# Optimization experiments

Hardware: AMD Instinct MI355X
Metric: run time of the kernel (lower is better)

Reference implementation:

```python
import jax, jax.numpy as jnp
import numpy as np

B = 512
EPS = 1e-5


def _coords():
    # cvt_coord(i) = [(i//5 - 2)/2, (i%5 - 2)/2] on a 5x5 grid
    c = np.array([[(i // 5 - 2) / 2.0, (i % 5 - 2) / 2.0] for i in range(25)], dtype=np.float32)
    return jnp.asarray(c)  # [25, 2]


def setup_inputs() -> dict:
    key = jax.random.key(0)
    ks = jax.random.split(key, 32)
    d = {
        'img': jax.random.normal(ks[0], (B, 3, 75, 75), jnp.float32),
        'qst': jax.random.normal(ks[1], (B, 11), jnp.float32),
    }
    # conv backbone params
    cin = [3, 24, 24, 24]
    for l in range(4):
        d[f'conv_w{l+1}'] = jax.random.normal(ks[2 + l], (24, cin[l], 3, 3), jnp.float32) * 0.1
        d[f'conv_b{l+1}'] = jnp.zeros((24,), jnp.float32)
        d[f'bn_g{l+1}'] = 1.0 + 0.05 * jax.random.normal(ks[6 + l], (24,), jnp.float32)
        d[f'bn_b{l+1}'] = 0.05 * jax.random.normal(ks[10 + l], (24,), jnp.float32)
    # g MLP (63->256, 256->256 x3)
    d['g_w1'] = jax.random.normal(ks[14], (256, 63), jnp.float32) * 0.05
    d['g_b1'] = jnp.zeros((256,), jnp.float32)
    for l in (2, 3, 4):
        d[f'g_w{l}'] = jax.random.normal(ks[13 + l], (256, 256), jnp.float32) * 0.05
        d[f'g_b{l}'] = jnp.zeros((256,), jnp.float32)
    # f MLP and output head
    d['f_w1'] = jax.random.normal(ks[20], (256, 256), jnp.float32) * 0.05
    d['f_b1'] = jnp.zeros((256,), jnp.float32)
    d['fc2_w'] = jax.random.normal(ks[21], (256, 256), jnp.float32) * 0.05
    d['fc2_b'] = jnp.zeros((256,), jnp.float32)
    d['fc3_w'] = jax.random.normal(ks[22], (10, 256), jnp.float32) * 0.05
    d['fc3_b'] = jnp.zeros((10,), jnp.float32)
    return d


def _conv_bn(x, w, b, g, be):
    y = jax.lax.conv_general_dilated(x, w, (2, 2), [(1, 1), (1, 1)],
                                     dimension_numbers=('NCHW', 'OIHW', 'NCHW'))
    y = jax.nn.relu(y + b[None, :, None, None])
    # BatchNorm2d with batch statistics (training-mode forward)
    mu = jnp.mean(y, axis=(0, 2, 3), keepdims=True)
    var = jnp.var(y, axis=(0, 2, 3), keepdims=True)
    return (y - mu) * jax.lax.rsqrt(var + EPS) * g[None, :, None, None] + be[None, :, None, None]


def _lin(x, w, b):
    return x @ w.T + b


def reference(img, qst,
              conv_w1, conv_b1, bn_g1, bn_b1,
              conv_w2, conv_b2, bn_g2, bn_b2,
              conv_w3, conv_b3, bn_g3, bn_b3,
              conv_w4, conv_b4, bn_g4, bn_b4,
              g_w1, g_b1, g_w2, g_b2, g_w3, g_b3, g_w4, g_b4,
              f_w1, f_b1, fc2_w, fc2_b, fc3_w, fc3_b):
    x = _conv_bn(img, conv_w1, conv_b1, bn_g1, bn_b1)
    x = _conv_bn(x, conv_w2, conv_b2, bn_g2, bn_b2)
    x = _conv_bn(x, conv_w3, conv_b3, bn_g3, bn_b3)
    x = _conv_bn(x, conv_w4, conv_b4, bn_g4, bn_b4)  # [B, 24, 5, 5]
    mb = x.shape[0]
    x_flat = x.reshape(mb, 24, 25).transpose(0, 2, 1)  # [B, 25, 24]
    coords = jnp.broadcast_to(_coords()[None], (mb, 25, 2))
    x_flat = jnp.concatenate([x_flat, coords], axis=2)  # [B, 25, 26]
    # all-pairs: pair (p, q) -> concat(obj_q, obj_p, qst)
    xj = jnp.concatenate([x_flat, jnp.broadcast_to(qst[:, None, :], (mb, 25, 11))], axis=2)  # [B,25,37]
    x_i = jnp.broadcast_to(x_flat[:, None, :, :], (mb, 25, 25, 26))
    x_j = jnp.broadcast_to(xj[:, :, None, :], (mb, 25, 25, 37))
    x_full = jnp.concatenate([x_i, x_j], axis=3).reshape(mb * 625, 63)
    h = jax.nn.relu(_lin(x_full, g_w1, g_b1))
    h = jax.nn.relu(_lin(h, g_w2, g_b2))
    h = jax.nn.relu(_lin(h, g_w3, g_b3))
    h = jax.nn.relu(_lin(h, g_w4, g_b4))
    x_g = h.reshape(mb, 625, 256).sum(axis=1)  # [B, 256]
    x_f = jax.nn.relu(_lin(x_g, f_w1, f_b1))
    x_f = jax.nn.relu(_lin(x_f, fc2_w, fc2_b))  # (dropout omitted: eval/deterministic)
    logits = _lin(x_f, fc3_w, fc3_b)
    return jax.nn.log_softmax(logits, axis=-1)
```

## Files before the change

### kernel.cpp

```cpp
#include <hip/hip_runtime.h>
#include <hip/hip_bf16.h>

#define EPS 1e-5f

typedef _Float16 half_t;
typedef __attribute__((ext_vector_type(8))) _Float16 h16x8;
typedef __attribute__((ext_vector_type(4))) _Float16 h16x4;
typedef __attribute__((ext_vector_type(4))) float f32x4;

__device__ __forceinline__ float relu_f(float x) { return x > 0.f ? x : 0.f; }

#define OFF_Y1   0
#define OFF_Y2   17743872
#define OFF_Y3   22179840
#define OFF_Y4   23408640
#define OFF_ST   23715840
#define OFF_WHL  23718912
#define OFF_A    0
#define OFF_BV   3276800
#define OFF_XG   6553600
#define OFF_WHL2 8871936

__global__ __launch_bounds__(256) void k_prep(const float* w2, const float* w3,
                                              const float* w4, half_t* whl, float* stats) {
    int idx = blockIdx.x * 256 + threadIdx.x;
    if (idx < 3072) stats[idx] = 0.f;
    int l = idx >> 16, e = idx & 65535;
    const float* w = (l == 0) ? w2 : (l == 1) ? w3 : w4;
    float v = w[e];
    int c = e >> 8, k = e & 255;
    int o = ((c >> 4) * 8 + (k >> 5)) * 512 + ((k >> 3) & 3) * 128 + (c & 15) * 8 + (k & 7);
    whl[l * 65536 + o] = (half_t)v;
}

__global__ __launch_bounds__(256) void k_prep2(const float* w2, half_t* whl2) {
    int idx = blockIdx.x * 256 + threadIdx.x;
    int ntile = idx / 3584, r = idx % 3584;
    int ks = r / 512, w = r % 512;
    int quad = w / 128, l15 = (w >> 3) & 15, j = w & 7;
    int k = ks * 32 + quad * 8 + j;
    int oc = ntile * 16 + l15;
    float v = 0.f;
    if (k < 216 && oc < 24) {
        int tap = k / 24, ic = k % 24;
        v = w2[(oc * 24 + ic) * 9 + tap];
    }
    whl2[idx] = (half_t)v;
}

__global__ __launch_bounds__(256, 2) void k_conv1(const float* img, const float* w,
                                                  const float* bias, half_t* y1, float* ostats) {
    __shared__ float wl[648], bl[24], red[4][48];
    int tid = threadIdx.x;
    if (tid < 24) bl[tid] = bias[tid];
    for (int i = tid; i < 648; i += 256) wl[i] = w[i];
    __syncthreads();
    int idx = blockIdx.x * 256 + tid;
    int b2 = idx / 1444, rem = idx % 1444;
    int b0 = b2 * 2;
    int oh = rem / 38, ow = rem % 38;
    float acc0[24], acc1[24];
#pragma unroll
    for (int o = 0; o < 24; ++o) { acc0[o] = bl[o]; acc1[o] = bl[o]; }
    for (int ic = 0; ic < 3; ++ic) {
        float p0[9], p1[9];
#pragma unroll
        for (int kh = 0; kh < 3; ++kh) {
            int ih = oh * 2 - 1 + kh;
#pragma unroll
            for (int kw = 0; kw < 3; ++kw) {
                int iw = ow * 2 - 1 + kw;
                bool ok = (unsigned)ih < 75u && (unsigned)iw < 75u;
                p0[kh * 3 + kw] = ok ? img[((b0 * 3 + ic) * 75 + ih) * 75 + iw] : 0.f;
                p1[kh * 3 + kw] = ok ? img[(((b0 + 1) * 3 + ic) * 75 + ih) * 75 + iw] : 0.f;
            }
        }
#pragma unroll
        for (int o = 0; o < 24; ++o)
#pragma unroll
            for (int t = 0; t < 9; ++t) {
                float wv = wl[(o * 3 + ic) * 9 + t];
                acc0[o] += wv * p0[t];
                acc1[o] += wv * p1[t];
            }
    }
#pragma unroll
    for (int o = 0; o < 24; ++o) { acc0[o] = relu_f(acc0[o]); acc1[o] = relu_f(acc1[o]); }
#pragma unroll
    for (int g = 0; g < 3; ++g) {
        h16x8 a, c;
#pragma unroll
        for (int j = 0; j < 8; ++j) { a[j] = (half_t)acc0[g * 8 + j]; c[j] = (half_t)acc1[g * 8 + j]; }
        *(h16x8*)&y1[((long)(b0) * 1444 + rem) * 24 + g * 8] = a;
        *(h16x8*)&y1[((long)(b0 + 1) * 1444 + rem) * 24 + g * 8] = c;
    }
    int wave = tid >> 6;
#pragma unroll
    for (int o = 0; o < 24; ++o) {
        float v = acc0[o] + acc1[o];
        float v2 = acc0[o] * acc0[o] + acc1[o] * acc1[o];
#pragma unroll
        for (int off = 1; off < 64; off <<= 1) { v += __shfl_xor(v, off); v2 += __shfl_xor(v2, off); }
        if ((tid & 63) == 0) { red[wave][o] = v; red[wave][24 + o] = v2; }
    }
    __syncthreads();
    if (tid < 48)
        atomicAdd(&ostats[(blockIdx.x & 15) * 48 + tid],
                  red[0][tid] + red[1][tid] + red[2][tid] + red[3][tid]);
}

__global__ __launch_bounds__(256) void k_conv2(const half_t* yin, const half_t* whl2,
                                               const float* bias, const float* instats,
                                               const float* bng, const float* bnb,
                                               float* yout, float* ostats) {
    __shared__ half_t yL[34672];
    __shared__ half_t wf[7168];
    __shared__ float outL[8856];
    __shared__ float scs[24], shs[24], bl[24], red[4][48];
    int tid = threadIdx.x;
    int b = blockIdx.x;
    if (tid < 24) {
        float s = 0.f, s2 = 0.f;
#pragma unroll
        for (int k = 0; k < 16; ++k) { s += instats[k * 48 + tid]; s2 += instats[k * 48 + 24 + tid]; }
        float mu = s * (1.f / 739328.f);
        float var = s2 * (1.f / 739328.f) - mu * mu;
        float sca = bng[tid] * rsqrtf(var + EPS);
        scs[tid] = sca; shs[tid] = bnb[tid] - mu * sca;
        bl[tid] = bias[tid];
    }
    if (tid < 16) yL[34656 + tid] = (half_t)0.f;
    for (int i = tid; i < 896; i += 256)
        ((h16x8*)wf)[i] = ((const h16x8*)whl2)[i];
    __syncthreads();
    const half_t* ybase = yin + (long)b * 34656;
    for (int i = tid; i < 4332; i += 256) {
        h16x8 v = *(const h16x8*)&ybase[i * 8];
        int ch0 = (i % 3) * 8;
        h16x8 o;
#pragma unroll
        for (int j = 0; j < 8; ++j)
            o[j] = (half_t)((float)v[j] * scs[ch0 + j] + shs[ch0 + j]);
        *(h16x8*)&yL[i * 8] = o;
    }
    __syncthreads();
    int wv = tid >> 6, lane = tid & 63, quad = lane >> 4, l15 = lane & 15;
    float bb0 = bl[l15];
    float bb1 = (l15 < 8) ? bl[16 + l15] : 0.f;
    float s0 = 0.f, q0 = 0.f, s1 = 0.f, q1 = 0.f;
    int t0 = wv * 6, t1 = t0 + 6; if (t1 > 23) t1 = 23;
#pragma unroll 1
    for (int t = t0; t < t1; ++t) {
        int px0 = t * 16;
        int pxa = px0 + l15; if (pxa > 360) pxa = 360;
        int oh = pxa / 19, ow = pxa % 19;
        f32x4 a0 = (f32x4){0.f, 0.f, 0.f, 0.f};
        f32x4 a1 = (f32x4){0.f, 0.f, 0.f, 0.f};
#pragma unroll
        for (int ks = 0; ks < 7; ++ks) {
            int k0 = ks * 32 + quad * 8;
            int tap = k0 / 24, ic0 = k0 - tap * 24;
            int kh = tap / 3, kw = tap - kh * 3;
            int ih = oh * 2 - 1 + kh, iw = ow * 2 - 1 + kw;
            bool val = (tap < 9) && ((unsigned)ih < 38u) && ((unsigned)iw < 38u);
            int aoff = val ? ((ih * 38 + iw) * 24 + ic0) : 34656;
            h16x8 af = *(const h16x8*)&yL[aoff];
            h16x8 w0 = *(const h16x8*)&wf[ks * 512 + quad * 128 + l15 * 8];
            h16x8 w1 = *(const h16x8*)&wf[3584 + ks * 512 + quad * 128 + l15 * 8];
            a0 = __builtin_amdgcn_mfma_f32_16x16x32_f16(af, w0, a0, 0, 0, 0);
            a1 = __builtin_amdgcn_mfma_f32_16x16x32_f16(af, w1, a1, 0, 0, 0);
        }
#pragma unroll
        for (int v = 0; v < 4; ++v) {
            int p = px0 + quad * 4 + v;
            bool pv = p < 361;
            float x0 = relu_f(a0[v] + bb0);
            float x1 = relu_f(a1[v] + bb1);
            outL[l15 * 369 + p] = x0;
            if (l15 < 8) outL[(16 + l15) * 369 + p] = x1;
            if (pv) {
                s0 += x0; q0 += x0 * x0;
                if (l15 < 8) { s1 += x1; q1 += x1 * x1; }
            }
        }
    }
    s0 += __shfl_xor(s0, 16); s0 += __shfl_xor(s0, 32);
    q0 += __shfl_xor(q0, 16); q0 += __shfl_xor(q0, 32);
    s1 += __shfl_xor(s1, 16); s1 += __shfl_xor(s1, 32);
    q1 += __shfl_xor(q1, 16); q1 += __shfl_xor(q1, 32);
    if (quad == 0) {
        red[wv][l15] = s0; red[wv][24 + l15] = q0;
        if (l15 < 8) { red[wv][16 + l15] = s1; red[wv][40 + l15] = q1; }
    }
    __syncthreads();
    float* yo = yout + (long)b * 8664;
    for (int i = tid; i < 8664; i += 256) {
        int oc = i / 361, p = i - oc * 361;
        yo[i] = outL[oc * 369 + p];
    }
    if (tid < 48)
        atomicAdd(&ostats[(blockIdx.x & 15) * 48 + tid],
                  red[0][tid] + red[1][tid] + red[2][tid] + red[3][tid]);
}

__global__ __launch_bounds__(256) void k_conv(const float* yin, const float* w,
                                              const float* bias, const float* instats,
                                              const float* bng, const float* bnb,
                                              float* yout, float* ostats,
                                              int Hin, int Hout, float invN) {
    __shared__ float wl[5184], bl[24], sc[24], sh[24], red[4][48];
    int tid = threadIdx.x;
    if (tid < 24) {
        float s = 0.f, s2 = 0.f;
#pragma unroll
        for (int k = 0; k < 16; ++k) { s += instats[k * 48 + tid]; s2 += instats[k * 48 + 24 + tid]; }
        float mu = s * invN;
        float var = s2 * invN - mu * mu;
        float sca = bng[tid] * rsqrtf(var + EPS);
        sc[tid] = sca; sh[tid] = bnb[tid] - mu * sca;
        bl[tid] = bias[tid];
    }
    for (int i = tid; i < 5184; i += 256) wl[i] = w[i];
    __syncthreads();
    int idx = blockIdx.x * 256 + tid;
    int HWo = Hout * Hout;
    int b = idx / HWo, rem = idx % HWo;
    int oh = rem / Hout, ow = rem % Hout;
    float acc[24];
#pragma unroll
    for (int o = 0; o < 24; ++o) acc[o] = bl[o];
    for (int ic = 0; ic < 24; ++ic) {
        float patch[9];
        float scc = sc[ic], shc = sh[ic];
#pragma unroll
        for (int kh = 0; kh < 3; ++kh) {
            int ih = oh * 2 - 1 + kh;
#pragma unroll
            for (int kw = 0; kw < 3; ++kw) {
                int iw = ow * 2 - 1 + kw;
                bool ok = (unsigned)ih < (unsigned)Hin && (unsigned)iw < (unsigned)Hin;
                patch[kh * 3 + kw] = ok ? yin[((b * 24 + ic) * Hin + ih) * Hin + iw] * scc + shc : 0.f;
            }
        }
#pragma unroll
        for (int o = 0; o < 24; ++o)
#pragma unroll
            for (int t = 0; t < 9; ++t) acc[o] += wl[(o * 24 + ic) * 9 + t] * patch[t];
    }
    int wave = tid >> 6;
#pragma unroll
    for (int o = 0; o < 24; ++o) {
        acc[o] = relu_f(acc[o]);
        yout[(b * 24 + o) * HWo + rem] = acc[o];
        float v = acc[o], v2 = v * v;
#pragma unroll
        for (int off = 1; off < 64; off <<= 1) { v += __shfl_xor(v, off); v2 += __shfl_xor(v2, off); }
        if ((tid & 63) == 0) { red[wave][o] = v; red[wave][24 + o] = v2; }
    }
    __syncthreads();
    if (tid < 48)
        atomicAdd(&ostats[(blockIdx.x & 15) * 48 + tid],
                  red[0][tid] + red[1][tid] + red[2][tid] + red[3][tid]);
}

__global__ __launch_bounds__(256) void k_obj(const float* y4, const float* qst,
                                             const float* w1, const float* b1,
                                             const float* instats, const float* bng,
                                             const float* bnb, float* A, float* Bv, float* xg) {
    int b = blockIdx.x, tid = threadIdx.x;
    __shared__ float w1l[16128];
    __shared__ float objs[25][28];
    __shared__ float sc[24], sh[24], q[11];
    xg[b * 256 + tid] = 0.f;
    for (int i = tid; i < 16128; i += 256) w1l[i] = w1[i];
    if (tid < 24) {
        float s = 0.f, s2 = 0.f;
#pragma unroll
        for (int k = 0; k < 16; ++k) { s += instats[k * 48 + tid]; s2 += instats[k * 48 + 24 + tid]; }
        float mu = s * (1.f / 12800.f);
        float var = s2 * (1.f / 12800.f) - mu * mu;
        float sca = bng[tid] * rsqrtf(var + EPS);
        sc[tid] = sca; sh[tid] = bnb[tid] - mu * sca;
    }
    if (tid < 11) q[tid] = qst[b * 11 + tid];
    __syncthreads();
    for (int i = tid; i < 600; i += 256) {
        int c = i / 25, p = i % 25;
        objs[p][c] = y4[b * 600 + i] * sc[c] + sh[c];
    }
    if (tid < 25) { objs[tid][24] = ((tid / 5) - 2) * 0.5f; objs[tid][25] = ((tid % 5) - 2) * 0.5f; }
    __syncthreads();
    float wr[63];
#pragma unroll
    for (int k = 0; k < 63; ++k) wr[k] = w1l[tid * 63 + k];
    float qdot = b1[tid];
#pragma unroll
    for (int j = 0; j < 11; ++j) qdot += wr[52 + j] * q[j];
#pragma unroll 1
    for (int p = 0; p < 25; ++p) {
        float a = 0.f, bv = qdot;
#pragma unroll
        for (int k = 0; k < 26; ++k) { a += wr[k] * objs[p][k]; bv += wr[26 + k] * objs[p][k]; }
        A[(b * 25 + p) * 256 + tid] = a;
        Bv[(b * 25 + p) * 256 + tid] = bv;
    }
}

#define GSTEP(C0,C1,C2,C3,N0,N1,N2,N3,KS,LKS,DOLOAD) do {                                   \
    int ko = (KS) * 32 + quad * 8;                                                          \
    h16x8 b0 = *(const h16x8*)&hr[0 * 4224 + ko];                                           \
    h16x8 b1 = *(const h16x8*)&hr[1 * 4224 + ko];                                           \
    h16x8 b2 = *(const h16x8*)&hr[2 * 4224 + ko];                                           \
    h16x8 b3 = *(const h16x8*)&hr[3 * 4224 + ko];                                           \
    if (DOLOAD) {                                                                           \
        N0 = *(const h16x8*)&W[0 * 4096 + (LKS) * 512];                                     \
        N1 = *(const h16x8*)&W[1 * 4096 + (LKS) * 512];                                     \
        N2 = *(const h16x8*)&W[2 * 4096 + (LKS) * 512];                                     \
        N3 = *(const h16x8*)&W[3 * 4096 + (LKS) * 512];                                     \
    }                                                                                       \
    __builtin_amdgcn_s_setprio(1);                                                          \
    acc[0][0] = __builtin_amdgcn_mfma_f32_16x16x32_f16(C0, b0, acc[0][0], 0, 0, 0);         \
    acc[1][0] = __builtin_amdgcn_mfma_f32_16x16x32_f16(C1, b0, acc[1][0], 0, 0, 0);         \
    acc[2][0] = __builtin_amdgcn_mfma_f32_16x16x32_f16(C2, b0, acc[2][0], 0, 0, 0);         \
    acc[3][0] = __builtin_amdgcn_mfma_f32_16x16x32_f16(C3, b0, acc[3][0], 0, 0, 0);         \
    acc[0][1] = __builtin_amdgcn_mfma_f32_16x16x32_f16(C0, b1, acc[0][1], 0, 0, 0);         \
    acc[1][1] = __builtin_amdgcn_mfma_f32_16x16x32_f16(C1, b1, acc[1][1], 0, 0, 0);         \
    acc[2][1] = __builtin_amdgcn_mfma_f32_16x16x32_f16(C2, b1, acc[2][1], 0, 0, 0);         \
    acc[3][1] = __builtin_amdgcn_mfma_f32_16x16x32_f16(C3, b1, acc[3][1], 0, 0, 0);         \
    acc[0][2] = __builtin_amdgcn_mfma_f32_16x16x32_f16(C0, b2, acc[0][2], 0, 0, 0);         \
    acc[1][2] = __builtin_amdgcn_mfma_f32_16x16x32_f16(C1, b2, acc[1][2], 0, 0, 0);         \
    acc[2][2] = __builtin_amdgcn_mfma_f32_16x16x32_f16(C2, b2, acc[2][2], 0, 0, 0);         \
    acc[3][2] = __builtin_amdgcn_mfma_f32_16x16x32_f16(C3, b2, acc[3][2], 0, 0, 0);         \
    acc[0][3] = __builtin_amdgcn_mfma_f32_16x16x32_f16(C0, b3, acc[0][3], 0, 0, 0);         \
    acc[1][3] = __builtin_amdgcn_mfma_f32_16x16x32_f16(C1, b3, acc[1][3], 0, 0, 0);         \
    acc[2][3] = __builtin_amdgcn_mfma_f32_16x16x32_f16(C2, b3, acc[2][3], 0, 0, 0);         \
    acc[3][3] = __builtin_amdgcn_mfma_f32_16x16x32_f16(C3, b3, acc[3][3], 0, 0, 0);         \
    __builtin_amdgcn_s_setprio(0);                                                          \
} while (0)

__global__ __launch_bounds__(256, 3) void k_g(const float* A, const float* Bv, const half_t* whl,
                                              const float* gb2, const float* gb3,
                                              const float* gb4, float* xg) {
    __shared__ alignas(16) half_t h[64 * 264];
    __shared__ float biasL[3][256];
    int tid = threadIdx.x;
    int lb = (blockIdx.x & 7) * 640 + (blockIdx.x >> 3);
    int b = lb / 10, t = lb % 10;
    int r0 = t * 64;
    int rmax = 625 - r0; if (rmax > 64) rmax = 64;
    biasL[0][tid] = gb2[tid];
    biasL[1][tid] = gb3[tid];
    biasL[2][tid] = gb4[tid];
    const float* Ab = A + b * 6400;
    const float* Bb = Bv + b * 6400;
#pragma unroll
    for (int it = 0; it < 16; ++it) {
        int r = it * 4 + (tid >> 6);
        int rs = __builtin_amdgcn_readfirstlane(r);
        int pr = r0 + rs; if (pr > 624) pr = 624;
        int i = pr % 25, j = pr / 25;
        int c4 = (tid & 63) << 2;
        float4 av = *(const float4*)&Ab[i * 256 + c4];
        float4 bv = *(const float4*)&Bb[j * 256 + c4];
        h16x4 hv = {(half_t)relu_f(av.x + bv.x), (half_t)relu_f(av.y + bv.y),
                    (half_t)relu_f(av.z + bv.z), (half_t)relu_f(av.w + bv.w)};
        *(h16x4*)&h[r * 264 + c4] = hv;
    }
    __syncthreads();
    int cg = tid >> 6, lane = tid & 63;
    int quad = lane >> 4, l15 = lane & 15;
    const half_t* hr = h + l15 * 264;
    const half_t* Wl = whl + (cg * 4) * 8 * 512 + lane * 8;
#pragma unroll 1
    for (int layer = 0; layer < 3; ++layer) {
        const half_t* W = Wl + layer * 65536;
        f32x4 acc[4][4];
#pragma unroll
        for (int mi = 0; mi < 4; ++mi)
#pragma unroll
            for (int nt = 0; nt < 4; ++nt) acc[mi][nt] = (f32x4){0.f, 0.f, 0.f, 0.f};
        h16x8 wA0 = *(const h16x8*)&W[0 * 4096];
        h16x8 wA1 = *(const h16x8*)&W[1 * 4096];
        h16x8 wA2 = *(const h16x8*)&W[2 * 4096];
        h16x8 wA3 = *(const h16x8*)&W[3 * 4096];
        h16x8 wB0 = *(const h16x8*)&W[0 * 4096 + 512];
        h16x8 wB1 = *(const h16x8*)&W[1 * 4096 + 512];
        h16x8 wB2 = *(const h16x8*)&W[2 * 4096 + 512];
        h16x8 wB3 = *(const h16x8*)&W[3 * 4096 + 512];
        h16x8 wC0, wC1, wC2, wC3;
        GSTEP(wA0, wA1, wA2, wA3, wC0, wC1, wC2, wC3, 0, 2, 1);
        GSTEP(wB0, wB1, wB2, wB3, wA0, wA1, wA2, wA3, 1, 3, 1);
        GSTEP(wC0, wC1, wC2, wC3, wB0, wB1, wB2, wB3, 2, 4, 1);
        GSTEP(wA0, wA1, wA2, wA3, wC0, wC1, wC2, wC3, 3, 5, 1);
        GSTEP(wB0, wB1, wB2, wB3, wA0, wA1, wA2, wA3, 4, 6, 1);
        GSTEP(wC0, wC1, wC2, wC3, wB0, wB1, wB2, wB3, 5, 7, 1);
        GSTEP(wA0, wA1, wA2, wA3, wA0, wA1, wA2, wA3, 6, 0, 0);
        GSTEP(wB0, wB1, wB2, wB3, wB0, wB1, wB2, wB3, 7, 0, 0);
        __syncthreads();
        if (layer < 2) {
#pragma unroll
            for (int mi = 0; mi < 4; ++mi) {
                int c0 = cg * 64 + mi * 16 + quad * 4;
#pragma unroll
                for (int nt = 0; nt < 4; ++nt) {
                    int row = nt * 16 + l15;
                    h16x4 hv;
#pragma unroll
                    for (int v = 0; v < 4; ++v)
                        hv[v] = (half_t)relu_f(acc[mi][nt][v] + biasL[layer][c0 + v]);
                    *(h16x4*)&h[row * 264 + c0] = hv;
                }
            }
            __syncthreads();
        } else {
#pragma unroll
            for (int mi = 0; mi < 4; ++mi) {
                int c0 = cg * 64 + mi * 16 + quad * 4;
#pragma unroll
                for (int v = 0; v < 4; ++v) {
                    float s = 0.f;
#pragma unroll
                    for (int nt = 0; nt < 4; ++nt) {
                        int row = nt * 16 + l15;
                        float x = relu_f(acc[mi][nt][v] + biasL[2][c0 + v]);
                        if (row < rmax) s += x;
                    }
                    s += __shfl_xor(s, 1);
                    s += __shfl_xor(s, 2);
                    s += __shfl_xor(s, 4);
                    s += __shfl_xor(s, 8);
                    if (l15 == 0) atomicAdd(&xg[b * 256 + c0 + v], s);
                }
            }
        }
    }
}

__global__ __launch_bounds__(256) void k_f(const float* xg, const float* fw1, const float* fb1,
                                           const float* fw2, const float* fb2,
                                           const float* fw3, const float* fb3, float* out) {
    int b0 = blockIdx.x * 2, tid = threadIdx.x;
    __shared__ float xb[2][256], h1[2][256], l10[2][10], red[2];
    xb[0][tid] = xg[b0 * 256 + tid];
    xb[1][tid] = xg[(b0 + 1) * 256 + tid];
    __syncthreads();
    float s0 = fb1[tid], s1 = s0;
    {
        const float4* wr = (const float4*)&fw1[tid * 256];
        const float4* x0 = (const float4*)xb[0];
        const float4* x1 = (const float4*)xb[1];
#pragma unroll 8
        for (int k = 0; k < 64; ++k) {
            float4 w = wr[k], a = x0[k], c = x1[k];
            s0 += w.x * a.x + w.y * a.y + w.z * a.z + w.w * a.w;
            s1 += w.x * c.x + w.y * c.y + w.z * c.z + w.w * c.w;
        }
    }
    h1[0][tid] = relu_f(s0);
    h1[1][tid] = relu_f(s1);
    __syncthreads();
    s0 = fb2[tid]; s1 = s0;
    {
        const float4* wr = (const float4*)&fw2[tid * 256];
        const float4* x0 = (const float4*)h1[0];
        const float4* x1 = (const float4*)h1[1];
#pragma unroll 8
        for (int k = 0; k < 64; ++k) {
            float4 w = wr[k], a = x0[k], c = x1[k];
            s0 += w.x * a.x + w.y * a.y + w.z * a.z + w.w * a.w;
            s1 += w.x * c.x + w.y * c.y + w.z * c.z + w.w * c.w;
        }
    }
    __syncthreads();
    xb[0][tid] = relu_f(s0);
    xb[1][tid] = relu_f(s1);
    __syncthreads();
    if (tid < 20) {
        int bb = tid / 10, o = tid % 10;
        float v = fb3[o];
        const float4* wr = (const float4*)&fw3[o * 256];
        const float4* hv = (const float4*)xb[bb];
#pragma unroll 8
        for (int k = 0; k < 64; ++k) {
            float4 w = wr[k], x = hv[k];
            v += w.x * x.x + w.y * x.y + w.z * x.z + w.w * x.w;
        }
        l10[bb][o] = v;
    }
    __syncthreads();
    if (tid < 2) {
        float m = l10[tid][0];
        for (int i = 1; i < 10; ++i) m = fmaxf(m, l10[tid][i]);
        float e = 0.f;
        for (int i = 0; i < 10; ++i) e += expf(l10[tid][i] - m);
        red[tid] = m + logf(e);
    }
    __syncthreads();
    if (tid < 20) {
        int bb = tid / 10, o = tid % 10;
        out[(b0 + bb) * 10 + o] = l10[bb][o] - red[bb];
    }
}

extern "C" void kernel_launch(void* const* d_in, const int* in_sizes, int n_in,
                              void* d_out, int out_size, void* d_ws, size_t ws_size,
                              hipStream_t stream) {
    const float* img = (const float*)d_in[0];
    const float* qst = (const float*)d_in[1];
    const float* cw[4] = {(const float*)d_in[2], (const float*)d_in[6],
                          (const float*)d_in[10], (const float*)d_in[14]};
    const float* cb[4] = {(const float*)d_in[3], (const float*)d_in[7],
                          (const float*)d_in[11], (const float*)d_in[15]};
    const float* bg[4] = {(const float*)d_in[4], (const float*)d_in[8],
                          (const float*)d_in[12], (const float*)d_in[16]};
    const float* bb[4] = {(const float*)d_in[5], (const float*)d_in[9],
                          (const float*)d_in[13], (const float*)d_in[17]};
    const float* gw1 = (const float*)d_in[18];
    const float* gb1 = (const float*)d_in[19];
    const float* gw2 = (const float*)d_in[20];
    const float* gb2 = (const float*)d_in[21];
    const float* gw3 = (const float*)d_in[22];
    const float* gb3 = (const float*)d_in[23];
    const float* gw4 = (const float*)d_in[24];
    const float* gb4 = (const float*)d_in[25];
    const float* fw1 = (const float*)d_in[26];
    const float* fb1 = (const float*)d_in[27];
    const float* fw2 = (const float*)d_in[28];
    const float* fb2 = (const float*)d_in[29];
    const float* fw3 = (const float*)d_in[30];
    const float* fb3 = (const float*)d_in[31];

    float* ws = (float*)d_ws;
    half_t* y1 = (half_t*)(ws + OFF_Y1);
    float* y2 = ws + OFF_Y2;
    float* y3 = ws + OFF_Y3;
    float* y4 = ws + OFF_Y4;
    float* st = ws + OFF_ST;
    half_t* whl = (half_t*)(ws + OFF_WHL);
    half_t* whl2 = (half_t*)(ws + OFF_WHL2);
    float* A = ws + OFF_A;
    float* Bv = ws + OFF_BV;
    float* xg = ws + OFF_XG;
    float* out = (float*)d_out;

    k_prep<<<768, 256, 0, stream>>>(gw2, gw3, gw4, whl, st);
    k_prep2<<<28, 256, 0, stream>>>(cw[1], whl2);
    k_conv1<<<1444, 256, 0, stream>>>(img, cw[0], cb[0], y1, st + 0 * 768);
    k_conv2<<<512, 256, 0, stream>>>(y1, whl2, cb[1], st + 0 * 768, bg[0], bb[0], y2,
                                     st + 1 * 768);
    k_conv<<<200, 256, 0, stream>>>(y2, cw[2], cb[2], st + 1 * 768, bg[1], bb[1], y3,
                                    st + 2 * 768, 19, 10, 1.f / 184832.f);
    k_conv<<<50, 256, 0, stream>>>(y3, cw[3], cb[3], st + 2 * 768, bg[2], bb[2], y4,
                                   st + 3 * 768, 10, 5, 1.f / 51200.f);
    k_obj<<<512, 256, 0, stream>>>(y4, qst, gw1, gb1, st + 3 * 768, bg[3], bb[3], A, Bv, xg);
    k_g<<<5120, 256, 0, stream>>>(A, Bv, whl, gb2, gb3, gb4, xg);
    k_f<<<256, 256, 0, stream>>>(xg, fw1, fb1, fw2, fb2, fw3, fb3, out);
}
```

Baseline: 517.4 us.

## Split conv2 by row halves, shrink conv3/4 blocks, merge prep kernels

Folds k_prep2 into k_prep to drop one launch. Splits k_conv2 into two blocks per image, each covering half the output rows with halo rows staged in LDS, and writes outputs straight to global instead of through an LDS staging buffer. This cuts LDS use and doubles the block count. Relaunches conv3/conv4 with smaller blocks (128 and 64 threads) for more parallelism, vectorizes the w1 load in k_obj, and raises k_g occupancy to 4 blocks per CU. The trade-offs are uncoalesced direct stores in conv2 and register pressure from the tighter k_g launch bound.

```diff
diff --git a/kernel.cpp b/kernel.cpp
--- a/kernel.cpp
+++ b/kernel.cpp
@@ -22,9 +22,23 @@
 #define OFF_WHL2 8871936
 
 __global__ __launch_bounds__(256) void k_prep(const float* w2, const float* w3,
-                                              const float* w4, half_t* whl, float* stats) {
+                                              const float* w4, half_t* whl, float* stats,
+                                              const float* cw2, half_t* whl2) {
     int idx = blockIdx.x * 256 + threadIdx.x;
     if (idx < 3072) stats[idx] = 0.f;
+    if (blockIdx.x < 28) {
+        int ntile = idx / 3584, r = idx % 3584;
+        int ks = r / 512, w = r % 512;
+        int quad = w / 128, l15 = (w >> 3) & 15, j = w & 7;
+        int k = ks * 32 + quad * 8 + j;
+        int oc = ntile * 16 + l15;
+        float v = 0.f;
+        if (k < 216 && oc < 24) {
+            int tap = k / 24, ic = k % 24;
+            v = cw2[(oc * 24 + ic) * 9 + tap];
+        }
+        whl2[idx] = (half_t)v;
+    }
     int l = idx >> 16, e = idx & 65535;
     const float* w = (l == 0) ? w2 : (l == 1) ? w3 : w4;
     float v = w[e];
@@ -33,21 +47,6 @@
     whl[l * 65536 + o] = (half_t)v;
 }
 
-__global__ __launch_bounds__(256) void k_prep2(const float* w2, half_t* whl2) {
-    int idx = blockIdx.x * 256 + threadIdx.x;
-    int ntile = idx / 3584, r = idx % 3584;
-    int ks = r / 512, w = r % 512;
-    int quad = w / 128, l15 = (w >> 3) & 15, j = w & 7;
-    int k = ks * 32 + quad * 8 + j;
-    int oc = ntile * 16 + l15;
-    float v = 0.f;
-    if (k < 216 && oc < 24) {
-        int tap = k / 24, ic = k % 24;
-        v = w2[(oc * 24 + ic) * 9 + tap];
-    }
-    whl2[idx] = (half_t)v;
-}
-
 __global__ __launch_bounds__(256, 2) void k_conv1(const float* img, const float* w,
                                                   const float* bias, half_t* y1, float* ostats) {
     __shared__ float wl[648], bl[24], red[4][48];
@@ -113,12 +112,15 @@
                                                const float* bias, const float* instats,
                                                const float* bng, const float* bnb,
                                                float* yout, float* ostats) {
-    __shared__ half_t yL[34672];
+    __shared__ half_t yL[19168];
     __shared__ half_t wf[7168];
-    __shared__ float outL[8856];
     __shared__ float scs[24], shs[24], bl[24], red[4][48];
     int tid = threadIdx.x;
-    int b = blockIdx.x;
+    int b = blockIdx.x >> 1, hh = blockIdx.x & 1;
+    int oh0 = hh * 10;
+    int NR = hh ? 9 : 10;
+    int NPX = NR * 19;
+    int ihbase = oh0 * 2 - 1;
     if (tid < 24) {
         float s = 0.f, s2 = 0.f;
 #pragma unroll
@@ -129,18 +131,25 @@
         scs[tid] = sca; shs[tid] = bnb[tid] - mu * sca;
         bl[tid] = bias[tid];
     }
-    if (tid < 16) yL[34656 + tid] = (half_t)0.f;
+    if (tid < 16) yL[19152 + tid] = (half_t)0.f;
     for (int i = tid; i < 896; i += 256)
         ((h16x8*)wf)[i] = ((const h16x8*)whl2)[i];
     __syncthreads();
     const half_t* ybase = yin + (long)b * 34656;
-    for (int i = tid; i < 4332; i += 256) {
-        h16x8 v = *(const h16x8*)&ybase[i * 8];
-        int ch0 = (i % 3) * 8;
+    for (int i = tid; i < 2394; i += 256) {
+        int li = i / 114, rem = i - li * 114;
+        int ih = ihbase + li;
         h16x8 o;
-#pragma unroll
-        for (int j = 0; j < 8; ++j)
-            o[j] = (half_t)((float)v[j] * scs[ch0 + j] + shs[ch0 + j]);
+        if ((unsigned)ih < 38u) {
+            h16x8 v = *(const h16x8*)&ybase[(ih * 114 + rem) * 8];
+            int ch0 = (rem % 3) * 8;
+#pragma unroll
+            for (int j = 0; j < 8; ++j)
+                o[j] = (half_t)((float)v[j] * scs[ch0 + j] + shs[ch0 + j]);
+        } else {
+#pragma unroll
+            for (int j = 0; j < 8; ++j) o[j] = (half_t)0.f;
+        }
         *(h16x8*)&yL[i * 8] = o;
     }
     __syncthreads();
@@ -148,12 +157,12 @@
     float bb0 = bl[l15];
     float bb1 = (l15 < 8) ? bl[16 + l15] : 0.f;
     float s0 = 0.f, q0 = 0.f, s1 = 0.f, q1 = 0.f;
-    int t0 = wv * 6, t1 = t0 + 6; if (t1 > 23) t1 = 23;
+    int ntiles = (NPX + 15) >> 4;
 #pragma unroll 1
-    for (int t = t0; t < t1; ++t) {
+    for (int t = wv; t < ntiles; t += 4) {
         int px0 = t * 16;
-        int pxa = px0 + l15; if (pxa > 360) pxa = 360;
-        int oh = pxa / 19, ow = pxa % 19;
+        int pxa = px0 + l15; if (pxa > NPX - 1) pxa = NPX - 1;
+        int lr = pxa / 19, ow = pxa % 19;
         f32x4 a0 = (f32x4){0.f, 0.f, 0.f, 0.f};
         f32x4 a1 = (f32x4){0.f, 0.f, 0.f, 0.f};
 #pragma unroll
@@ -161,9 +170,11 @@
             int k0 = ks * 32 + quad * 8;
             int tap = k0 / 24, ic0 = k0 - tap * 24;
             int kh = tap / 3, kw = tap - kh * 3;
-            int ih = oh * 2 - 1 + kh, iw = ow * 2 - 1 + kw;
-            bool val = (tap < 9) && ((unsigned)ih < 38u) && ((unsigned)iw < 38u);
-            int aoff = val ? ((ih * 38 + iw) * 24 + ic0) : 34656;
+            int li = 2 * lr + kh;
+            int ihg = ihbase + li;
+            int iw = ow * 2 - 1 + kw;
+            bool val = (tap < 9) && ((unsigned)ihg < 38u) && ((unsigned)iw < 38u);
+            int aoff = val ? ((li * 38 + iw) * 24 + ic0) : 19152;
             h16x8 af = *(const h16x8*)&yL[aoff];
             h16x8 w0 = *(const h16x8*)&wf[ks * 512 + quad * 128 + l15 * 8];
             h16x8 w1 = *(const h16x8*)&wf[3584 + ks * 512 + quad * 128 + l15 * 8];
@@ -173,14 +184,16 @@
 #pragma unroll
         for (int v = 0; v < 4; ++v) {
             int p = px0 + quad * 4 + v;
-            bool pv = p < 361;
-            float x0 = relu_f(a0[v] + bb0);
-            float x1 = relu_f(a1[v] + bb1);
-            outL[l15 * 369 + p] = x0;
-            if (l15 < 8) outL[(16 + l15) * 369 + p] = x1;
-            if (pv) {
+            if (p < NPX) {
+                int pg = oh0 * 19 + p;
+                float x0 = relu_f(a0[v] + bb0);
+                yout[((long)b * 24 + l15) * 361 + pg] = x0;
                 s0 += x0; q0 += x0 * x0;
-                if (l15 < 8) { s1 += x1; q1 += x1 * x1; }
+                if (l15 < 8) {
+                    float x1 = relu_f(a1[v] + bb1);
+                    yout[((long)b * 24 + 16 + l15) * 361 + pg] = x1;
+                    s1 += x1; q1 += x1 * x1;
+                }
             }
         }
     }
@@ -193,11 +206,6 @@
         if (l15 < 8) { red[wv][16 + l15] = s1; red[wv][40 + l15] = q1; }
     }
     __syncthreads();
-    float* yo = yout + (long)b * 8664;
-    for (int i = tid; i < 8664; i += 256) {
-        int oc = i / 361, p = i - oc * 361;
-        yo[i] = outL[oc * 369 + p];
-    }
     if (tid < 48)
         atomicAdd(&ostats[(blockIdx.x & 15) * 48 + tid],
                   red[0][tid] + red[1][tid] + red[2][tid] + red[3][tid]);
@@ -210,6 +218,7 @@
                                               int Hin, int Hout, float invN) {
     __shared__ float wl[5184], bl[24], sc[24], sh[24], red[4][48];
     int tid = threadIdx.x;
+    int bdim = blockDim.x;
     if (tid < 24) {
         float s = 0.f, s2 = 0.f;
 #pragma unroll
@@ -220,9 +229,9 @@
         sc[tid] = sca; sh[tid] = bnb[tid] - mu * sca;
         bl[tid] = bias[tid];
     }
-    for (int i = tid; i < 5184; i += 256) wl[i] = w[i];
-    __syncthreads();
-    int idx = blockIdx.x * 256 + tid;
+    for (int i = tid; i < 5184; i += bdim) wl[i] = w[i];
+    __syncthreads();
+    int idx = blockIdx.x * bdim + tid;
     int HWo = Hout * Hout;
     int b = idx / HWo, rem = idx % HWo;
     int oh = rem / Hout, ow = rem % Hout;
@@ -248,6 +257,7 @@
             for (int t = 0; t < 9; ++t) acc[o] += wl[(o * 24 + ic) * 9 + t] * patch[t];
     }
     int wave = tid >> 6;
+    int nw = bdim >> 6;
 #pragma unroll
     for (int o = 0; o < 24; ++o) {
         acc[o] = relu_f(acc[o]);
@@ -258,9 +268,11 @@
         if ((tid & 63) == 0) { red[wave][o] = v; red[wave][24 + o] = v2; }
     }
     __syncthreads();
-    if (tid < 48)
-        atomicAdd(&ostats[(blockIdx.x & 15) * 48 + tid],
-                  red[0][tid] + red[1][tid] + red[2][tid] + red[3][tid]);
+    if (tid < 48) {
+        float s = red[0][tid];
+        for (int w2 = 1; w2 < nw; ++w2) s += red[w2][tid];
+        atomicAdd(&ostats[(blockIdx.x & 15) * 48 + tid], s);
+    }
 }
 
 __global__ __launch_bounds__(256) void k_obj(const float* y4, const float* qst,
@@ -272,7 +284,8 @@
     __shared__ float objs[25][28];
     __shared__ float sc[24], sh[24], q[11];
     xg[b * 256 + tid] = 0.f;
-    for (int i = tid; i < 16128; i += 256) w1l[i] = w1[i];
+    for (int i = tid; i < 4032; i += 256)
+        ((float4*)w1l)[i] = ((const float4*)w1)[i];
     if (tid < 24) {
         float s = 0.f, s2 = 0.f;
 #pragma unroll
@@ -338,7 +351,7 @@
     __builtin_amdgcn_s_setprio(0);                                                          \
 } while (0)
 
-__global__ __launch_bounds__(256, 3) void k_g(const float* A, const float* Bv, const half_t* whl,
+__global__ __launch_bounds__(256, 4) void k_g(const float* A, const float* Bv, const half_t* whl,
                                               const float* gb2, const float* gb3,
                                               const float* gb4, float* xg) {
     __shared__ alignas(16) half_t h[64 * 264];
@@ -543,14 +556,13 @@
     float* xg = ws + OFF_XG;
     float* out = (float*)d_out;
 
-    k_prep<<<768, 256, 0, stream>>>(gw2, gw3, gw4, whl, st);
-    k_prep2<<<28, 256, 0, stream>>>(cw[1], whl2);
+    k_prep<<<768, 256, 0, stream>>>(gw2, gw3, gw4, whl, st, cw[1], whl2);
     k_conv1<<<1444, 256, 0, stream>>>(img, cw[0], cb[0], y1, st + 0 * 768);
-    k_conv2<<<512, 256, 0, stream>>>(y1, whl2, cb[1], st + 0 * 768, bg[0], bb[0], y2,
-                                     st + 1 * 768);
-    k_conv<<<200, 256, 0, stream>>>(y2, cw[2], cb[2], st + 1 * 768, bg[1], bb[1], y3,
+    k_conv2<<<1024, 256, 0, stream>>>(y1, whl2, cb[1], st + 0 * 768, bg[0], bb[0], y2,
+                                      st + 1 * 768);
+    k_conv<<<400, 128, 0, stream>>>(y2, cw[2], cb[2], st + 1 * 768, bg[1], bb[1], y3,
                                     st + 2 * 768, 19, 10, 1.f / 184832.f);
-    k_conv<<<50, 256, 0, stream>>>(y3, cw[3], cb[3], st + 2 * 768, bg[2], bb[2], y4,
+    k_conv<<<200, 64, 0, stream>>>(y3, cw[3], cb[3], st + 2 * 768, bg[2], bb[2], y4,
                                    st + 3 * 768, 10, 5, 1.f / 51200.f);
     k_obj<<<512, 256, 0, stream>>>(y4, qst, gw1, gb1, st + 3 * 768, bg[3], bb[3], A, Bv, xg);
     k_g<<<5120, 256, 0, stream>>>(A, Bv, whl, gb2, gb3, gb4, xg);
```

After: 766.9 us. +48.2%, slower.
